# Optimization experiments

Measured on AMD Instinct MI355X. Metric: run time of the kernel, lower is better.

## Reference

```python
import jax, jax.numpy as jnp
import numpy as np

B, L = 8, 16384
H = 64          # num_channel
N2 = 32         # s4_hidden_size // 2 complex conjugate-pair modes
DEPTH = 4       # model_depth
NLAYERS = 1 + DEPTH  # number of DSSM layers
EPS = 1e-5


def setup_inputs() -> dict:
    key = jax.random.key(0)
    ks = jax.random.split(key, 12)
    x = jax.random.normal(ks[0], (B, L), dtype=jnp.float32)
    # input linear 1 -> H
    w_in = jax.random.normal(ks[1], (H,), dtype=jnp.float32)
    b_in = jax.random.normal(ks[2], (H,), dtype=jnp.float32) * 0.1
    # hidden linears H -> H
    w_mid = jax.random.normal(ks[3], (DEPTH, H, H), dtype=jnp.float32) / np.sqrt(H)
    b_mid = jax.random.normal(ks[4], (DEPTH, H), dtype=jnp.float32) * 0.1
    # output linear H -> 1
    w_out = jax.random.normal(ks[5], (H,), dtype=jnp.float32) / np.sqrt(H)
    b_out = jax.random.normal(ks[6], (), dtype=jnp.float32) * 0.1
    # S4D / DSSM parameters (stacked over the 5 SSM layers)
    log_dt = (jax.random.uniform(ks[7], (NLAYERS, H), dtype=jnp.float32)
              * (np.log(0.1) - np.log(0.001)) + np.log(0.001))
    log_A_real = jnp.log(0.5 * jnp.ones((NLAYERS, H, N2), dtype=jnp.float32))
    A_imag = jnp.pi * jnp.broadcast_to(jnp.arange(N2, dtype=jnp.float32), (NLAYERS, H, N2))
    C_re = jax.random.normal(ks[8], (NLAYERS, H, N2), dtype=jnp.float32)
    C_im = jax.random.normal(ks[9], (NLAYERS, H, N2), dtype=jnp.float32)
    D = jax.random.normal(ks[10], (NLAYERS, H), dtype=jnp.float32)
    return {"x": x, "w_in": w_in, "b_in": b_in, "w_mid": w_mid, "b_mid": b_mid,
            "w_out": w_out, "b_out": b_out, "log_dt": log_dt,
            "log_A_real": log_A_real, "A_imag": A_imag,
            "C_re": C_re, "C_im": C_im, "D": D}


def _dssm(u, log_dt, log_A_real, A_imag, C_re, C_im, D):
    # u: [B, H, L]; diagonal SSM applied as FFT convolution (S4D ZOH kernel)
    Lq = u.shape[-1]
    dt = jnp.exp(log_dt)                      # [H]
    A = -jnp.exp(log_A_real) + 1j * A_imag    # [H, N2]
    dtA = A * dt[:, None]                     # [H, N2]
    C_eff = (C_re + 1j * C_im) * (jnp.exp(dtA) - 1.0) / A
    # Vandermonde: exp(dtA * l) for l in [0, L)
    V = jnp.exp(dtA[:, :, None] * jnp.arange(Lq, dtype=jnp.float32))  # [H, N2, L]
    k = 2.0 * jnp.einsum('hn,hnl->hl', C_eff, V).real                # [H, L]
    uf = jnp.fft.rfft(u, n=2 * Lq)
    kf = jnp.fft.rfft(k, n=2 * Lq)
    y = jnp.fft.irfft(uf * kf, n=2 * Lq)[..., :Lq]
    return y + u * D[:, None]


def reference(x, w_in, b_in, w_mid, b_mid, w_out, b_out,
              log_dt, log_A_real, A_imag, C_re, C_im, D):
    # side chain: Abs -> Decibel -> Linear(1,H) -> tanh -> [DSSM -> tanh] ...
    s = 20.0 * jnp.log10(jnp.abs(x) + EPS)            # [B, L]
    h = jnp.tanh(s[..., None] * w_in + b_in)          # [B, L, H]
    h = jnp.tanh(_dssm(h.transpose(0, 2, 1), log_dt[0], log_A_real[0],
                       A_imag[0], C_re[0], C_im[0], D[0]).transpose(0, 2, 1))
    for i in range(DEPTH):
        h = jnp.tanh(jnp.einsum('blh,oh->blo', h, w_mid[i]) + b_mid[i])
        j = i + 1
        h = jnp.tanh(_dssm(h.transpose(0, 2, 1), log_dt[j], log_A_real[j],
                           A_imag[j], C_re[j], C_im[j], D[j]).transpose(0, 2, 1))
    g = jnp.einsum('blh,h->bl', h, w_out) + b_out      # [B, L]
    g = jnp.power(10.0, g / 20.0)                      # Amplitude (dB -> linear)
    return x * g
```

## Files before the change

kernel.cpp:

```cpp
#include <hip/hip_runtime.h>
#include <math.h>

#define Bq 8
#define Lq 16384
#define Hq 64
#define N2q 32
#define NLAYERSq 5

typedef _Float16 f16x8 __attribute__((ext_vector_type(8)));
typedef _Float16 f16x4 __attribute__((ext_vector_type(4)));
typedef float    f32x4 __attribute__((ext_vector_type(4)));

#define MFMA16F(a, b, c) __builtin_amdgcn_mfma_f32_16x16x32_f16(a, b, c, 0, 0, 0)

#define UT_OFF    0
#define SS_OFF    32768
#define SMEM_SZ   50176
#define YST_OFF   0

#define WT_OFF_B   0
#define WP_OFF_B   163840
#define A2_OFF_B   (163840 + 5242880)
#define W16_OFF_B  (163840 + 5242880 + 15728640)
#define U_OFF_B    (163840 + 5242880 + 15728640 + 32768)

__device__ __forceinline__ float fast_tanh(float y) {
    float e = __expf(2.0f * y);
    return 1.0f - 2.0f * __builtin_amdgcn_rcpf(e + 1.0f);
}

__global__ __launch_bounds__(256)
void k_prep(const float* __restrict__ log_dt, const float* __restrict__ log_A_real,
            const float* __restrict__ A_imag, const float* __restrict__ C_re,
            const float* __restrict__ C_im, const float* __restrict__ Dvec,
            const float* __restrict__ w_mid,
            float* __restrict__ wT_tab, _Float16* __restrict__ Wp,
            _Float16* __restrict__ A2, _Float16* __restrict__ W16) {
    __shared__ float Pr[129][33], Pi[129][33];
    __shared__ float cre[32], cim[32], Kv[128];
    __shared__ double sdAr[32], sdAi[32];
    const int ph = blockIdx.x >> 2;
    const int qt = blockIdx.x & 3;
    const int tid = threadIdx.x;

    if (qt == 0 && ph < 256 && tid < 64) {
        int e = ph * 64 + tid;
        W16[e] = (_Float16)w_mid[e];
    }

    if (tid < 32) {
        int n = tid;
        int pidx = ph * N2q + n;
        double dt  = exp((double)log_dt[ph]);
        double aRe = -exp((double)log_A_real[pidx]);
        double aIm = (double)A_imag[pidx];
        double dAr = aRe * dt, dAi = aIm * dt;
        sdAr[n] = dAr; sdAi[n] = dAi;
        double er  = exp(dAr);
        double wre = er * cos(dAi), wim = er * sin(dAi);
        double Er = wre - 1.0, Ei = wim;
        double inv = 1.0 / (aRe * aRe + aIm * aIm);
        double Fr = (Er * aRe + Ei * aIm) * inv;
        double Fi = (Ei * aRe - Er * aIm) * inv;
        double Cr = (double)C_re[pidx], Ci = (double)C_im[pidx];
        cre[n] = (float)(2.0 * (Cr * Fr - Ci * Fi));
        cim[n] = (float)(2.0 * (Cr * Fi + Ci * Fr));
        if (qt == 0) {
            double qr = wre, qi = wim;
            #pragma unroll
            for (int s = 0; s < 7; s++) {
                double nr = qr * qr - qi * qi;
                qi = 2.0 * qr * qi; qr = nr;
            }
            float wTr = (float)qr, wTi = (float)qi;
            #pragma unroll
            for (int s = 0; s < 4; s++) {
                double nr = qr * qr - qi * qi;
                qi = 2.0 * qr * qi; qr = nr;
            }
            float* wt = wT_tab + ph * 128 + n * 4;
            wt[0] = wTr; wt[1] = wTi; wt[2] = (float)qr; wt[3] = (float)qi;
        }
    }
    __syncthreads();

    const double TWO_PI  = 6.2831853071795864769;
    const double INV_2PI = 0.15915494309189533577;
    for (int e = tid; e < 129 * 32; e += 256) {
        int j = e >> 5, n = e & 31;
        double phd = (double)j * sdAi[n];
        double r   = fma(-TWO_PI, nearbyint(phd * INV_2PI), phd);
        float  mag = __expf((float)((double)j * sdAr[n]));
        float  rf  = (float)r;
        Pr[j][n] = mag * cosf(rf);
        Pi[j][n] = mag * sinf(rf);
    }
    __syncthreads();

    if (tid < 128) {
        int d = tid;
        float s = 0.f;
        #pragma unroll 8
        for (int n = 0; n < 32; n++)
            s += cre[n] * Pr[d][n] - cim[n] * Pi[d][n];
        if (d == 0) s += Dvec[ph];
        Kv[d] = s;
    }
    __syncthreads();

    {
        _Float16* wpb = Wp + (size_t)ph * 8192;
        int o = tid;
        int kk = (qt << 4) + (o >> 4);
        int l0 = (o & 15) * 8;
        f16x8 v;
        #pragma unroll
        for (int j = 0; j < 8; j++) {
            int l = l0 + j;
            v[j] = (_Float16)((kk < 32) ? Pr[127 - l][kk] : Pi[127 - l][kk - 32]);
        }
        *(f16x8*)(wpb + kk * 128 + l0) = v;
    }
    {
        _Float16* a2b = A2 + (size_t)ph * 24576;
        for (int o = tid; o < 768; o += 256) {
            int m  = (qt << 5) + (o / 24);
            int k0 = (o % 24) * 8;
            f16x8 v;
            #pragma unroll
            for (int j = 0; j < 8; j++) {
                int k = k0 + j;
                float f;
                if (k < 128) {
                    f = (k <= m) ? Kv[m - k] : 0.f;
                } else {
                    int kk = k - 128, n2 = kk & 31;
                    float pr = Pr[m + 1][n2], pi2 = Pi[m + 1][n2];
                    f = (kk < 32) ? (cre[n2] * pr - cim[n2] * pi2)
                                  : -(cre[n2] * pi2 + cim[n2] * pr);
                }
                v[j] = (_Float16)f;
            }
            *(f16x8*)(a2b + m * 192 + k0) = v;
        }
    }
}

__global__ __launch_bounds__(256, 3)
void k_scan(const float* __restrict__ x, _Float16* __restrict__ u16,
            const _Float16* __restrict__ Wp_all, const _Float16* __restrict__ A2_all,
            const float* __restrict__ wT_all, int layer,
            const float* __restrict__ w_in, const float* __restrict__ b_in) {
    extern __shared__ char smem[];
    char* UT = smem + UT_OFF;
    char* Sf = smem + SS_OFF;
    char* St = smem + SS_OFF;
    char* yst = smem + YST_OFF;

    const int bh = blockIdx.x;
    const int h  = bh & 63;
    const int tid = threadIdx.x;
    const int lane = tid & 63;
    const int wave = tid >> 6;
    const int ph = layer * 64 + h;
    const _Float16* Wp = Wp_all + (size_t)ph * 8192;
    const _Float16* A2 = A2_all + (size_t)ph * 24576;
    const float* wT4 = wT_all + ph * 128;
    _Float16* uu = u16 + ((size_t)bh << 14);

    const int rA = lane & 15;
    const int qA = lane >> 4;

    if (layer == 0) {
        const float* xb = x + ((size_t)(bh >> 6) << 14);
        const float wi = w_in[h], bi = b_in[h];
        for (int it = 0; it < 8; ++it) {
            int flat8 = (it * 256 + tid) * 8;
            int n = flat8 >> 7, k = flat8 & 127;
            float4 a = *(const float4*)(xb + flat8);
            float4 b = *(const float4*)(xb + flat8 + 4);
            float f[8] = {a.x, a.y, a.z, a.w, b.x, b.y, b.z, b.w};
            f16x8 hv;
            #pragma unroll
            for (int j = 0; j < 8; j++) {
                float s = 6.0205999132796239f * __log2f(fabsf(f[j]) + 1e-5f);
                hv[j] = (_Float16)fast_tanh(fmaf(s, wi, bi));
            }
            *(f16x8*)(UT + n * 256 + ((k * 2) ^ ((n & 7) << 4))) = hv;
        }
    } else {
        for (int it = 0; it < 8; ++it) {
            int flat8 = (it * 256 + tid) * 8;
            int n = flat8 >> 7, k = flat8 & 127;
            f16x8 hv = *(const f16x8*)(uu + flat8);
            *(f16x8*)(UT + n * 256 + ((k * 2) ^ ((n & 7) << 4))) = hv;
        }
    }
    __syncthreads();

    {
        f32x4 acc1[8];
        #pragma unroll
        for (int nt = 0; nt < 8; nt++) acc1[nt] = (f32x4){0.f, 0.f, 0.f, 0.f};
        for (int ks = 0; ks < 4; ks++) {
            f16x8 af = *(const f16x8*)(Wp + (wave * 16 + rA) * 128 + ks * 32 + qA * 8);
            #pragma unroll
            for (int nt = 0; nt < 8; nt++) {
                int n = nt * 16 + rA;
                f16x8 bv = *(const f16x8*)(UT + n * 256 + ((ks * 64 + qA * 16) ^ ((n & 7) << 4)));
                acc1[nt] = MFMA16F(af, bv, acc1[nt]);
            }
        }
        #pragma unroll
        for (int nt = 0; nt < 8; nt++) {
            int c = nt * 16 + rA;
            #pragma unroll
            for (int r = 0; r < 4; r++)
                *(_Float16*)(Sf + (wave * 16 + qA * 4 + r) * 272 + c * 2) = (_Float16)acc1[nt][r];
        }
    }
    __syncthreads();

    {
        const int sn = tid >> 3;
        const int ss = tid & 7;
        const float wTr = wT4[sn * 4 + 0], wTi = wT4[sn * 4 + 1];
        float fr[16], fi[16];
        {
            f16x8 a0 = *(const f16x8*)(Sf + sn * 272 + ss * 32);
            f16x8 a1 = *(const f16x8*)(Sf + sn * 272 + ss * 32 + 16);
            f16x8 b0 = *(const f16x8*)(Sf + (sn + 32) * 272 + ss * 32);
            f16x8 b1 = *(const f16x8*)(Sf + (sn + 32) * 272 + ss * 32 + 16);
            #pragma unroll
            for (int j = 0; j < 8; j++) {
                fr[j] = (float)a0[j]; fr[j + 8] = (float)a1[j];
                fi[j] = (float)b0[j]; fi[j + 8] = (float)b1[j];
            }
        }
        float Tr = 0.f, Ti = 0.f;
        #pragma unroll
        for (int i = 0; i < 16; i++) {
            float nTr = fmaf(wTr, Tr, fmaf(-wTi, Ti, fr[i]));
            Ti = fmaf(wTr, Ti, fmaf(wTi, Tr, fi[i]));
            Tr = nTr;
        }
        float gr = wT4[sn * 4 + 2], gi = wT4[sn * 4 + 3];
        #pragma unroll
        for (int s = 0; s < 3; s++) {
            float pr = __shfl_up(Tr, 1 << s, 8);
            float pi = __shfl_up(Ti, 1 << s, 8);
            if (ss >= (1 << s)) {
                Tr = fmaf(gr, pr, fmaf(-gi, pi, Tr));
                Ti = fmaf(gr, pi, fmaf(gi, pr, Ti));
            }
            float ngr = fmaf(gr, gr, -gi * gi);
            gi = 2.f * gr * gi; gr = ngr;
        }
        float Er_ = __shfl_up(Tr, 1, 8);
        float Ei_ = __shfl_up(Ti, 1, 8);
        if (ss == 0) { Er_ = 0.f; Ei_ = 0.f; }
        __syncthreads();
        float Gr = Er_, Gi = Ei_;
        #pragma unroll
        for (int i = 0; i < 16; i++) {
            int c = ss * 16 + i;
            int sw = (c & 7) << 4;
            *(_Float16*)(St + c * 128 + ((sn * 2) ^ sw))        = (_Float16)Gr;
            *(_Float16*)(St + c * 128 + (((sn + 32) * 2) ^ sw)) = (_Float16)Gi;
            float nGr = fmaf(wTr, Gr, fmaf(-wTi, Gi, fr[i]));
            Gi = fmaf(wTr, Gi, fmaf(wTi, Gr, fi[i]));
            Gr = nGr;
        }
    }
    __syncthreads();

    f32x4 acc[2][8];
    #pragma unroll
    for (int mi = 0; mi < 2; mi++)
        #pragma unroll
        for (int nt = 0; nt < 8; nt++) acc[mi][nt] = (f32x4){0.f, 0.f, 0.f, 0.f};
    #pragma unroll
    for (int mi = 0; mi < 2; mi++) {
        const _Float16* Arow = A2 + ((wave * 2 + mi) * 16 + rA) * 192;
        for (int ks = 0; ks < 4; ks++) {
            f16x8 af = *(const f16x8*)(Arow + ks * 32 + qA * 8);
            #pragma unroll
            for (int nt = 0; nt < 8; nt++) {
                int n = nt * 16 + rA;
                f16x8 bv = *(const f16x8*)(UT + n * 256 + ((ks * 64 + qA * 16) ^ ((n & 7) << 4)));
                acc[mi][nt] = MFMA16F(af, bv, acc[mi][nt]);
            }
        }
        #pragma unroll
        for (int ks2 = 0; ks2 < 2; ks2++) {
            f16x8 af = *(const f16x8*)(Arow + 128 + ks2 * 32 + qA * 8);
            #pragma unroll
            for (int nt = 0; nt < 8; nt++) {
                int c = nt * 16 + rA;
                f16x8 bv = *(const f16x8*)(St + c * 128 + ((ks2 * 64 + qA * 16) ^ ((c & 7) << 4)));
                acc[mi][nt] = MFMA16F(af, bv, acc[mi][nt]);
            }
        }
    }
    __syncthreads();

    #pragma unroll
    for (int mi = 0; mi < 2; mi++) {
        int m0 = (wave * 2 + mi) * 16 + qA * 4;
        #pragma unroll
        for (int nt = 0; nt < 8; nt++) {
            int c = nt * 16 + rA;
            f16x4 o;
            o[0] = (_Float16)fast_tanh(acc[mi][nt][0]);
            o[1] = (_Float16)fast_tanh(acc[mi][nt][1]);
            o[2] = (_Float16)fast_tanh(acc[mi][nt][2]);
            o[3] = (_Float16)fast_tanh(acc[mi][nt][3]);
            *(f16x4*)(yst + c * 272 + m0 * 2) = o;
        }
    }
    __syncthreads();
    for (int it = 0; it < 8; ++it) {
        int e = it * 256 + tid;
        int c = e >> 4, l8 = e & 15;
        f16x8 hv = *(const f16x8*)(yst + c * 272 + l8 * 16);
        *(f16x8*)(uu + c * 128 + l8 * 8) = hv;
    }
}

__global__ __launch_bounds__(256, 4)
void k_linear(_Float16* __restrict__ uio, const _Float16* __restrict__ W16,
              const float* __restrict__ bias) {
    __shared__ __align__(16) char lmem[33792];
    _Float16* Ul  = (_Float16*)lmem;
    _Float16* yst = (_Float16*)lmem;

    const int b   = blockIdx.y;
    const int l0  = blockIdx.x * 256;
    const int tid = threadIdx.x;
    const int lane = tid & 63;
    const int wave = tid >> 6;
    const int rA = lane & 15;
    const int qA = lane >> 4;

    _Float16* ub = uio + ((size_t)b << 20) + l0;

    for (int it = 0; it < 4; ++it) {
        int g  = it * 256 + tid;
        int hp = g >> 5;
        int l8 = g & 31;
        f16x8 v0 = *(const f16x8*)(ub + (size_t)(hp * 2)     * Lq + l8 * 8);
        f16x8 v1 = *(const f16x8*)(ub + (size_t)(hp * 2 + 1) * Lq + l8 * 8);
        const unsigned short* p0 = (const unsigned short*)&v0;
        const unsigned short* p1 = (const unsigned short*)&v1;
        int sw = (l8 & 7) << 4;
        #pragma unroll
        for (int j = 0; j < 8; j++) {
            unsigned int pk = (unsigned int)p0[j] | ((unsigned int)p1[j] << 16);
            *(unsigned int*)((char*)Ul + (l8 * 8 + j) * 128 + ((hp * 4) ^ sw)) = pk;
        }
    }
    __syncthreads();

    f32x4 acc[16];
    #pragma unroll
    for (int nt = 0; nt < 16; nt++) acc[nt] = (f32x4){0.f, 0.f, 0.f, 0.f};
    const _Float16* Wrow = W16 + (wave * 16 + rA) * 64;
    #pragma unroll
    for (int kf = 0; kf < 2; kf++) {
        f16x8 af = *(const f16x8*)(Wrow + kf * 32 + qA * 8);
        #pragma unroll
        for (int nt = 0; nt < 16; nt++) {
            int n = nt * 16 + rA;
            int sw = ((n >> 3) & 7) << 4;
            f16x8 bv = *(const f16x8*)((char*)Ul + n * 128 + ((kf * 64 + qA * 16) ^ sw));
            acc[nt] = MFMA16F(af, bv, acc[nt]);
        }
    }
    __syncthreads();

    {
        int ob = wave * 16 + qA * 4;
        float bo0 = bias[ob], bo1 = bias[ob + 1], bo2 = bias[ob + 2], bo3 = bias[ob + 3];
        #pragma unroll
        for (int nt = 0; nt < 16; nt++) {
            int l = nt * 16 + rA;
            yst[(ob + 0) * 264 + l] = (_Float16)fast_tanh(acc[nt][0] + bo0);
            yst[(ob + 1) * 264 + l] = (_Float16)fast_tanh(acc[nt][1] + bo1);
            yst[(ob + 2) * 264 + l] = (_Float16)fast_tanh(acc[nt][2] + bo2);
            yst[(ob + 3) * 264 + l] = (_Float16)fast_tanh(acc[nt][3] + bo3);
        }
    }
    __syncthreads();
    for (int it = 0; it < 8; ++it) {
        int e = it * 256 + tid;
        int o = e >> 5, l8 = e & 31;
        f16x8 hv = *(const f16x8*)(yst + o * 264 + l8 * 8);
        *(f16x8*)(ub + (size_t)o * Lq + l8 * 8) = hv;
    }
}

__global__ __launch_bounds__(256)
void k_out(const _Float16* __restrict__ u16, const float* __restrict__ x,
           const float* __restrict__ w_out, const float* __restrict__ b_out,
           float* __restrict__ out) {
    int idx = blockIdx.x * 256 + threadIdx.x;
    int b = idx >> 14;
    int l = idx & (Lq - 1);
    const _Float16* up = u16 + ((size_t)b << 20) + l;
    float acc = 0.f;
    #pragma unroll 8
    for (int hh = 0; hh < 64; ++hh)
        acc = fmaf(w_out[hh], (float)up[(size_t)hh << 14], acc);
    float g = acc + b_out[0];
    out[idx] = x[idx] * exp2f(g * 0.16609640474436812f);
}

extern "C" void kernel_launch(void* const* d_in, const int* in_sizes, int n_in,
                              void* d_out, int out_size, void* d_ws, size_t ws_size,
                              hipStream_t stream) {
    const float* x          = (const float*)d_in[0];
    const float* w_in       = (const float*)d_in[1];
    const float* b_in       = (const float*)d_in[2];
    const float* w_mid      = (const float*)d_in[3];
    const float* b_mid      = (const float*)d_in[4];
    const float* w_out      = (const float*)d_in[5];
    const float* b_out      = (const float*)d_in[6];
    const float* log_dt     = (const float*)d_in[7];
    const float* log_A_real = (const float*)d_in[8];
    const float* A_imag     = (const float*)d_in[9];
    const float* C_re       = (const float*)d_in[10];
    const float* C_im       = (const float*)d_in[11];
    const float* Dv         = (const float*)d_in[12];

    char* ws = (char*)d_ws;
    float*     wT_tab = (float*)(ws + WT_OFF_B);
    _Float16*  Wp     = (_Float16*)(ws + WP_OFF_B);
    _Float16*  A2     = (_Float16*)(ws + A2_OFF_B);
    _Float16*  W16    = (_Float16*)(ws + W16_OFF_B);
    _Float16*  u16    = (_Float16*)(ws + U_OFF_B);
    float* out = (float*)d_out;

    hipFuncSetAttribute((const void*)k_scan,
                        hipFuncAttributeMaxDynamicSharedMemorySize, SMEM_SZ);

    k_prep<<<NLAYERSq * Hq * 4, 256, 0, stream>>>(log_dt, log_A_real, A_imag,
                                                  C_re, C_im, Dv, w_mid,
                                                  wT_tab, Wp, A2, W16);
    for (int layer = 0; layer < NLAYERSq; layer++) {
        if (layer > 0)
            k_linear<<<dim3(Lq / 256, Bq), 256, 0, stream>>>(
                u16, W16 + (size_t)(layer - 1) * Hq * Hq, b_mid + (size_t)(layer - 1) * Hq);
        k_scan<<<Bq * Hq, 256, SMEM_SZ, stream>>>(x, u16, Wp, A2, wT_tab, layer,
                                                  w_in, b_in);
    }
    k_out<<<(Bq * Lq) / 256, 256, 0, stream>>>(u16, x, w_out, b_out, out);
}
```

Baseline: 175.7 us.

## Double k_scan block to 512 threads and split scan and MFMA work across eight waves

The chunked scan kernel now runs 512 threads per block instead of 256. Each wave handles fewer MFMA tiles: half the N tiles in the first projection and one M tile in the output GEMM. The chunk scan uses 16 lanes per mode with 8 elements each, so the inter-chunk stride table drops one squaring. The aim is more parallelism and less serial work per thread within a block, in exchange for fewer resident blocks per CU (launch bounds 512,2) and an extra shuffle step.

```diff
diff --git a/kernel.cpp b/kernel.cpp
--- a/kernel.cpp
+++ b/kernel.cpp
@@ -74,7 +74,7 @@
             }
             float wTr = (float)qr, wTi = (float)qi;
             #pragma unroll
-            for (int s = 0; s < 4; s++) {
+            for (int s = 0; s < 3; s++) {
                 double nr = qr * qr - qi * qi;
                 qi = 2.0 * qr * qi; qr = nr;
             }
@@ -146,7 +146,7 @@
     }
 }
 
-__global__ __launch_bounds__(256, 3)
+__global__ __launch_bounds__(512, 2)
 void k_scan(const float* __restrict__ x, _Float16* __restrict__ u16,
             const _Float16* __restrict__ Wp_all, const _Float16* __restrict__ A2_all,
             const float* __restrict__ wT_all, int layer,
@@ -174,8 +174,8 @@
     if (layer == 0) {
         const float* xb = x + ((size_t)(bh >> 6) << 14);
         const float wi = w_in[h], bi = b_in[h];
-        for (int it = 0; it < 8; ++it) {
-            int flat8 = (it * 256 + tid) * 8;
+        for (int it = 0; it < 4; ++it) {
+            int flat8 = (it * 512 + tid) * 8;
             int n = flat8 >> 7, k = flat8 & 127;
             float4 a = *(const float4*)(xb + flat8);
             float4 b = *(const float4*)(xb + flat8 + 4);
@@ -189,8 +189,8 @@
             *(f16x8*)(UT + n * 256 + ((k * 2) ^ ((n & 7) << 4))) = hv;
         }
     } else {
-        for (int it = 0; it < 8; ++it) {
-            int flat8 = (it * 256 + tid) * 8;
+        for (int it = 0; it < 4; ++it) {
+            int flat8 = (it * 512 + tid) * 8;
             int n = flat8 >> 7, k = flat8 & 127;
             f16x8 hv = *(const f16x8*)(uu + flat8);
             *(f16x8*)(UT + n * 256 + ((k * 2) ^ ((n & 7) << 4))) = hv;
@@ -199,56 +199,57 @@
     __syncthreads();
 
     {
-        f32x4 acc1[8];
-        #pragma unroll
-        for (int nt = 0; nt < 8; nt++) acc1[nt] = (f32x4){0.f, 0.f, 0.f, 0.f};
+        f32x4 acc1[4];
+        #pragma unroll
+        for (int nt = 0; nt < 4; nt++) acc1[nt] = (f32x4){0.f, 0.f, 0.f, 0.f};
+        const int mt1 = wave & 3;
+        const int nh  = (wave >> 2) * 4;
+        #pragma unroll
         for (int ks = 0; ks < 4; ks++) {
-            f16x8 af = *(const f16x8*)(Wp + (wave * 16 + rA) * 128 + ks * 32 + qA * 8);
-            #pragma unroll
-            for (int nt = 0; nt < 8; nt++) {
-                int n = nt * 16 + rA;
+            f16x8 af = *(const f16x8*)(Wp + (mt1 * 16 + rA) * 128 + ks * 32 + qA * 8);
+            #pragma unroll
+            for (int nt = 0; nt < 4; nt++) {
+                int n = (nh + nt) * 16 + rA;
                 f16x8 bv = *(const f16x8*)(UT + n * 256 + ((ks * 64 + qA * 16) ^ ((n & 7) << 4)));
                 acc1[nt] = MFMA16F(af, bv, acc1[nt]);
             }
         }
         #pragma unroll
-        for (int nt = 0; nt < 8; nt++) {
-            int c = nt * 16 + rA;
+        for (int nt = 0; nt < 4; nt++) {
+            int c = (nh + nt) * 16 + rA;
             #pragma unroll
             for (int r = 0; r < 4; r++)
-                *(_Float16*)(Sf + (wave * 16 + qA * 4 + r) * 272 + c * 2) = (_Float16)acc1[nt][r];
-        }
-    }
-    __syncthreads();
-
-    {
-        const int sn = tid >> 3;
-        const int ss = tid & 7;
+                *(_Float16*)(Sf + (mt1 * 16 + qA * 4 + r) * 272 + c * 2) = (_Float16)acc1[nt][r];
+        }
+    }
+    __syncthreads();
+
+    {
+        const int sn = tid >> 4;
+        const int ss = tid & 15;
         const float wTr = wT4[sn * 4 + 0], wTi = wT4[sn * 4 + 1];
-        float fr[16], fi[16];
+        float fr[8], fi[8];
         {
-            f16x8 a0 = *(const f16x8*)(Sf + sn * 272 + ss * 32);
-            f16x8 a1 = *(const f16x8*)(Sf + sn * 272 + ss * 32 + 16);
-            f16x8 b0 = *(const f16x8*)(Sf + (sn + 32) * 272 + ss * 32);
-            f16x8 b1 = *(const f16x8*)(Sf + (sn + 32) * 272 + ss * 32 + 16);
+            f16x8 a0 = *(const f16x8*)(Sf + sn * 272 + ss * 16);
+            f16x8 b0 = *(const f16x8*)(Sf + (sn + 32) * 272 + ss * 16);
             #pragma unroll
             for (int j = 0; j < 8; j++) {
-                fr[j] = (float)a0[j]; fr[j + 8] = (float)a1[j];
-                fi[j] = (float)b0[j]; fi[j + 8] = (float)b1[j];
+                fr[j] = (float)a0[j];
+                fi[j] = (float)b0[j];
             }
         }
         float Tr = 0.f, Ti = 0.f;
         #pragma unroll
-        for (int i = 0; i < 16; i++) {
+        for (int i = 0; i < 8; i++) {
             float nTr = fmaf(wTr, Tr, fmaf(-wTi, Ti, fr[i]));
             Ti = fmaf(wTr, Ti, fmaf(wTi, Tr, fi[i]));
             Tr = nTr;
         }
         float gr = wT4[sn * 4 + 2], gi = wT4[sn * 4 + 3];
         #pragma unroll
-        for (int s = 0; s < 3; s++) {
-            float pr = __shfl_up(Tr, 1 << s, 8);
-            float pi = __shfl_up(Ti, 1 << s, 8);
+        for (int s = 0; s < 4; s++) {
+            float pr = __shfl_up(Tr, 1 << s, 16);
+            float pi = __shfl_up(Ti, 1 << s, 16);
             if (ss >= (1 << s)) {
                 Tr = fmaf(gr, pr, fmaf(-gi, pi, Tr));
                 Ti = fmaf(gr, pi, fmaf(gi, pr, Ti));
@@ -256,14 +257,14 @@
             float ngr = fmaf(gr, gr, -gi * gi);
             gi = 2.f * gr * gi; gr = ngr;
         }
-        float Er_ = __shfl_up(Tr, 1, 8);
-        float Ei_ = __shfl_up(Ti, 1, 8);
+        float Er_ = __shfl_up(Tr, 1, 16);
+        float Ei_ = __shfl_up(Ti, 1, 16);
         if (ss == 0) { Er_ = 0.f; Ei_ = 0.f; }
         __syncthreads();
         float Gr = Er_, Gi = Ei_;
         #pragma unroll
-        for (int i = 0; i < 16; i++) {
-            int c = ss * 16 + i;
+        for (int i = 0; i < 8; i++) {
+            int c = ss * 8 + i;
             int sw = (c & 7) << 4;
             *(_Float16*)(St + c * 128 + ((sn * 2) ^ sw))        = (_Float16)Gr;
             *(_Float16*)(St + c * 128 + (((sn + 32) * 2) ^ sw)) = (_Float16)Gi;
@@ -274,21 +275,19 @@
     }
     __syncthreads();
 
-    f32x4 acc[2][8];
+    f32x4 acc[8];
     #pragma unroll
-    for (int mi = 0; mi < 2; mi++)
-        #pragma unroll
-        for (int nt = 0; nt < 8; nt++) acc[mi][nt] = (f32x4){0.f, 0.f, 0.f, 0.f};
-    #pragma unroll
-    for (int mi = 0; mi < 2; mi++) {
-        const _Float16* Arow = A2 + ((wave * 2 + mi) * 16 + rA) * 192;
+    for (int nt = 0; nt < 8; nt++) acc[nt] = (f32x4){0.f, 0.f, 0.f, 0.f};
+    {
+        const _Float16* Arow = A2 + (wave * 16 + rA) * 192;
+        #pragma unroll
         for (int ks = 0; ks < 4; ks++) {
             f16x8 af = *(const f16x8*)(Arow + ks * 32 + qA * 8);
             #pragma unroll
             for (int nt = 0; nt < 8; nt++) {
                 int n = nt * 16 + rA;
                 f16x8 bv = *(const f16x8*)(UT + n * 256 + ((ks * 64 + qA * 16) ^ ((n & 7) << 4)));
-                acc[mi][nt] = MFMA16F(af, bv, acc[mi][nt]);
+                acc[nt] = MFMA16F(af, bv, acc[nt]);
             }
         }
         #pragma unroll
@@ -298,29 +297,28 @@
             for (int nt = 0; nt < 8; nt++) {
                 int c = nt * 16 + rA;
                 f16x8 bv = *(const f16x8*)(St + c * 128 + ((ks2 * 64 + qA * 16) ^ ((c & 7) << 4)));
-                acc[mi][nt] = MFMA16F(af, bv, acc[mi][nt]);
-            }
-        }
-    }
-    __syncthreads();
-
-    #pragma unroll
-    for (int mi = 0; mi < 2; mi++) {
-        int m0 = (wave * 2 + mi) * 16 + qA * 4;
+                acc[nt] = MFMA16F(af, bv, acc[nt]);
+            }
+        }
+    }
+    __syncthreads();
+
+    {
+        int m0 = wave * 16 + qA * 4;
         #pragma unroll
         for (int nt = 0; nt < 8; nt++) {
             int c = nt * 16 + rA;
             f16x4 o;
-            o[0] = (_Float16)fast_tanh(acc[mi][nt][0]);
-            o[1] = (_Float16)fast_tanh(acc[mi][nt][1]);
-            o[2] = (_Float16)fast_tanh(acc[mi][nt][2]);
-            o[3] = (_Float16)fast_tanh(acc[mi][nt][3]);
+            o[0] = (_Float16)fast_tanh(acc[nt][0]);
+            o[1] = (_Float16)fast_tanh(acc[nt][1]);
+            o[2] = (_Float16)fast_tanh(acc[nt][2]);
+            o[3] = (_Float16)fast_tanh(acc[nt][3]);
             *(f16x4*)(yst + c * 272 + m0 * 2) = o;
         }
     }
     __syncthreads();
-    for (int it = 0; it < 8; ++it) {
-        int e = it * 256 + tid;
+    for (int it = 0; it < 4; ++it) {
+        int e = it * 512 + tid;
         int c = e >> 4, l8 = e & 15;
         f16x8 hv = *(const f16x8*)(yst + c * 272 + l8 * 16);
         *(f16x8*)(uu + c * 128 + l8 * 8) = hv;
@@ -450,7 +448,7 @@
         if (layer > 0)
             k_linear<<<dim3(Lq / 256, Bq), 256, 0, stream>>>(
                 u16, W16 + (size_t)(layer - 1) * Hq * Hq, b_mid + (size_t)(layer - 1) * Hq);
-        k_scan<<<Bq * Hq, 256, SMEM_SZ, stream>>>(x, u16, Wp, A2, wT_tab, layer,
+        k_scan<<<Bq * Hq, 512, SMEM_SZ, stream>>>(x, u16, Wp, A2, wT_tab, layer,
                                                   w_in, b_in);
     }
     k_out<<<(Bq * Lq) / 256, 256, 0, stream>>>(u16, x, w_out, b_out, out);
```

After: 190.7 us. 1.08x slower.
